# Kernel optimization log

Hardware: AMD Instinct MI355X
Metric: run time of the kernel (lower is better)

The kernel has to match this reference:

```python
import jax, jax.numpy as jnp
import numpy as np

X_DIM = 64
HIDDEN = 256
B = 64
T = 2048


def setup_inputs() -> dict:
    key = jax.random.key(0)
    k1, k2, k3, k4 = jax.random.split(key, 4)
    s = 1.0 / np.sqrt(HIDDEN)  # equinox LSTMCell uniform init scale
    x_seq = jax.random.normal(k1, (B, T, X_DIM), dtype=jnp.float32)
    w_ih = jax.random.uniform(k2, (4 * HIDDEN, X_DIM), minval=-s, maxval=s, dtype=jnp.float32)
    w_hh = jax.random.uniform(k3, (4 * HIDDEN, HIDDEN), minval=-s, maxval=s, dtype=jnp.float32)
    bias = jax.random.uniform(k4, (4 * HIDDEN,), minval=-s, maxval=s, dtype=jnp.float32)
    return {"x_seq": x_seq, "w_ih": w_ih, "w_hh": w_hh, "bias": bias}


def reference(x_seq, w_ih, w_hh, bias):
    # x_seq: (B, T, x_dim) -> h_seq: (B, T, H). Gate order i,f,g,o (equinox/torch).
    Bsz, Tlen, _ = x_seq.shape
    H = w_hh.shape[1]
    h0 = jnp.zeros((Bsz, H), dtype=x_seq.dtype)
    c0 = jnp.zeros((Bsz, H), dtype=x_seq.dtype)

    def step(carry, x_t):
        h, c = carry
        z = x_t @ w_ih.T + h @ w_hh.T + bias  # (B, 4H)
        i, f, g, o = jnp.split(z, 4, axis=-1)
        i = jax.nn.sigmoid(i)
        f = jax.nn.sigmoid(f)
        g = jnp.tanh(g)
        o = jax.nn.sigmoid(o)
        c = f * c + i * g
        h = o * jnp.tanh(c)
        return (h, c), h

    (_, _), hs = jax.lax.scan(step, (h0, c0), x_seq.transpose(1, 0, 2))  # hs: (T, B, H)
    return hs.transpose(1, 0, 2)
```

## Files before the change

### kernel.cpp

```cpp
#include <hip/hip_runtime.h>

#define XD    64
#define HID   256
#define G4    1024
#define TLEN  2048
#define BATCH 64
#define NPART 8
#define UPB   32
#define CPB   128
#define TSTRIDE 16

typedef unsigned int uint;

__device__ __forceinline__ float sigmf(float x) {
    return 1.0f / (1.0f + __expf(-x));
}
__device__ __forceinline__ float tanhfast(float x) {
    return 1.0f - 2.0f / (1.0f + __expf(2.0f * x));
}

__device__ __forceinline__ uint2 ld_pair_sc0(const uint2* p) {
    uint2 r;
    asm volatile("global_load_dwordx2 %0, %1, off sc0 nt\n\ts_waitcnt vmcnt(0)"
                 : "=v"(r) : "v"(p) : "memory");
    return r;
}
__device__ __forceinline__ void st_pair_sc0(uint2* p, uint2 v) {
    asm volatile("global_store_dwordx2 %0, %1, off sc0" :: "v"(p), "v"(v) : "memory");
}
__device__ __forceinline__ uint2 ld_pair_dev(const uint2* p) {
    unsigned long long u = __hip_atomic_load((const unsigned long long*)p,
                                             __ATOMIC_RELAXED, __HIP_MEMORY_SCOPE_AGENT);
    uint2 r; r.x = (uint)(u & 0xffffffffu); r.y = (uint)(u >> 32); return r;
}
__device__ __forceinline__ void st_pair_dev(uint2* p, uint2 v) {
    unsigned long long u = ((unsigned long long)v.y << 32) | (unsigned long long)v.x;
    __hip_atomic_store((unsigned long long*)p, u, __ATOMIC_RELAXED, __HIP_MEMORY_SCOPE_AGENT);
}

__global__ void init_ws(unsigned long long* __restrict__ pairs, int* __restrict__ tok) {
    const int i = blockIdx.x * 256 + threadIdx.x;
    pairs[i] = 0ULL;
    pairs[BATCH * HID + i] = 0ULL;
    if (threadIdx.x < TSTRIDE) tok[blockIdx.x * TSTRIDE + threadIdx.x] = 0;
}

__global__ __launch_bounds__(256, 2)
void lstm_par(const float* __restrict__ x,
              const float* __restrict__ wih,
              const float* __restrict__ whh,
              const float* __restrict__ bias,
              float* __restrict__ out,
              uint2* __restrict__ pairs,
              int* __restrict__ tok)
{
    const int b    = blockIdx.x & 63;
    const int part = blockIdx.x >> 6;
    const int tid  = threadIdx.x;
    const int lane = tid & 63;
    const int wv   = tid >> 6;
    const int s    = tid >> 5;
    const int cq   = tid & 31;

    __shared__ __align__(16) float vec[XD + HID];
    __shared__ __align__(16) float zp[4][CPB];
    __shared__ int fastsh;

    float4 w4[40];
    {
        int jr[4];
        #pragma unroll
        for (int k = 0; k < 4; ++k) {
            const int c = 4 * cq + k;
            jr[k] = (c >> 5) * 256 + part * UPB + (c & 31);
        }
        #pragma unroll
        for (int e = 0; e < 40; ++e) {
            const int ge = s * 40 + e;
            float v0, v1, v2, v3;
            if (ge < XD) {
                v0 = wih[jr[0] * XD + ge]; v1 = wih[jr[1] * XD + ge];
                v2 = wih[jr[2] * XD + ge]; v3 = wih[jr[3] * XD + ge];
            } else {
                const int he = ge - XD;
                v0 = whh[jr[0] * HID + he]; v1 = whh[jr[1] * HID + he];
                v2 = whh[jr[2] * HID + he]; v3 = whh[jr[3] * HID + he];
            }
            w4[e] = make_float4(v0, v1, v2, v3);
        }
    }
    float bi = 0.f, bf = 0.f, bg = 0.f, bo = 0.f;
    if (tid < UPB) {
        const int gj = part * UPB + tid;
        bi = bias[gj]; bf = bias[256 + gj]; bg = bias[512 + gj]; bo = bias[768 + gj];
    }

    {
        int xcc;
        asm volatile("s_getreg_b32 %0, hwreg(HW_REG_XCC_ID)" : "=s"(xcc));
        xcc &= 15;
        int* tb = tok + b * TSTRIDE;
        if (tid == 0)
            __hip_atomic_store(tb + part, 256 + xcc, __ATOMIC_RELEASE,
                               __HIP_MEMORY_SCOPE_AGENT);
        if (tid < 64) {
            const int ln = tid & 7;
            int v = 0, guard = 0;
            for (;;) {
                v = __hip_atomic_load(tb + ln, __ATOMIC_RELAXED,
                                      __HIP_MEMORY_SCOPE_AGENT);
                if (__all(v >= 256)) break;
                __builtin_amdgcn_s_sleep(2);
                if (++guard > 200000) break;
            }
            const int ok = __all(v >= 256);
            const int v0 = __shfl(v, 0);
            const int eq = (ok && __all(v == v0)) ? 1 : 0;
            if (tid == 0) fastsh = eq;
        }
        __syncthreads();
    }
    const bool fast = (fastsh != 0);

    uint2* __restrict__ pb0 = pairs + (size_t)b * HID;
    uint2* __restrict__ pb1 = pairs + (size_t)(BATCH + b) * HID;
    const float* __restrict__ xb = x + (size_t)b * TLEN * XD;
    float* __restrict__ ob = out + (size_t)b * TLEN * HID;

    float cst = 0.0f;
    float xreg = (tid < XD) ? xb[tid] : 0.0f;

    for (int t = 0; t < TLEN; ++t) {
        if (t > 0) {
            const uint2* src = ((t & 1) ? pb0 : pb1) + tid;
            uint2 pr;
            int it = 0;
            for (;;) {
                pr = (fast && it < 4096) ? ld_pair_sc0(src) : ld_pair_dev(src);
                if (pr.y == (uint)t) break;
                __builtin_amdgcn_s_sleep(1);
                if (++it > 100000) break;
            }
            vec[XD + tid] = __uint_as_float(pr.x);
        } else {
            vec[XD + tid] = 0.0f;
        }
        if (tid < XD) vec[tid] = xreg;
        __syncthreads();

        if (t + 1 < TLEN && tid < XD) xreg = xb[(size_t)(t + 1) * XD + tid];

        float4 acc = make_float4(0.f, 0.f, 0.f, 0.f);
        const float4* vb = (const float4*)(vec + 40 * s);
        #pragma unroll
        for (int i = 0; i < 10; ++i) {
            const float4 v = vb[i];
            #define FMA1(R, VE)                              \
                acc.x = fmaf(w4[4*i + R].x, (VE), acc.x);    \
                acc.y = fmaf(w4[4*i + R].y, (VE), acc.y);    \
                acc.z = fmaf(w4[4*i + R].z, (VE), acc.z);    \
                acc.w = fmaf(w4[4*i + R].w, (VE), acc.w);
            FMA1(0, v.x) FMA1(1, v.y) FMA1(2, v.z) FMA1(3, v.w)
            #undef FMA1
        }
        acc.x += __shfl_xor(acc.x, 32);
        acc.y += __shfl_xor(acc.y, 32);
        acc.z += __shfl_xor(acc.z, 32);
        acc.w += __shfl_xor(acc.w, 32);
        if (lane < 32) *(float4*)(&zp[wv][4 * lane]) = acc;
        __syncthreads();

        if (tid < UPB) {
            float zi = bi, zf = bf, zg = bg, zo = bo;
            #pragma unroll
            for (int w2 = 0; w2 < 4; ++w2) {
                zi += zp[w2][tid];
                zf += zp[w2][32 + tid];
                zg += zp[w2][64 + tid];
                zo += zp[w2][96 + tid];
            }
            const float ig = sigmf(zi);
            const float fg = sigmf(zf);
            const float gg = tanhfast(zg);
            const float og = sigmf(zo);
            cst = fg * cst + ig * gg;
            const float h = og * tanhfast(cst);
            uint2 pv; pv.x = __float_as_uint(h); pv.y = (uint)(t + 1);
            uint2* dst = ((t & 1) ? pb1 : pb0) + part * UPB + tid;
            if (fast) st_pair_sc0(dst, pv);
            else      st_pair_dev(dst, pv);
            ob[(size_t)t * HID + part * UPB + tid] = h;
        }
    }
}

extern "C" void kernel_launch(void* const* d_in, const int* in_sizes, int n_in,
                              void* d_out, int out_size, void* d_ws, size_t ws_size,
                              hipStream_t stream) {
    const float* x    = (const float*)d_in[0];
    const float* wih  = (const float*)d_in[1];
    const float* whh  = (const float*)d_in[2];
    const float* bias = (const float*)d_in[3];
    float* out = (float*)d_out;

    uint2* pairs = (uint2*)d_ws;
    int*   tok   = (int*)((char*)d_ws + (size_t)2 * BATCH * HID * sizeof(uint2));

    hipLaunchKernelGGL(init_ws, dim3(BATCH), dim3(256), 0, stream,
                       (unsigned long long*)d_ws, tok);
    hipLaunchKernelGGL(lstm_par, dim3(BATCH * NPART), dim3(256), 0, stream,
                       x, wih, whh, bias, out, pairs, tok);
}
```

Baseline: 2.759 ms.

## Interleave two batch chains per block to hide cross-block latency

Each block now handles two batch elements (A and B) in alternation using the same register-resident weights. This halves the grid from 512 to 256 blocks and sets launch bounds to 1 block per SM. While chain A's h values travel between blocks, the block computes chain B, which is meant to hide the inter-block exchange latency. The cost is twice the serial compute per block per timestep, and the sync groups now span two batches.

```diff
diff --git a/kernel.cpp b/kernel.cpp
--- a/kernel.cpp
+++ b/kernel.cpp
@@ -6,6 +6,7 @@
 #define TLEN  2048
 #define BATCH 64
 #define NPART 8
+#define NGRP  32
 #define UPB   32
 #define CPB   128
 #define TSTRIDE 16
@@ -45,7 +46,7 @@
     if (threadIdx.x < TSTRIDE) tok[blockIdx.x * TSTRIDE + threadIdx.x] = 0;
 }
 
-__global__ __launch_bounds__(256, 2)
+__global__ __launch_bounds__(256, 1)
 void lstm_par(const float* __restrict__ x,
               const float* __restrict__ wih,
               const float* __restrict__ whh,
@@ -54,16 +55,18 @@
               uint2* __restrict__ pairs,
               int* __restrict__ tok)
 {
-    const int b    = blockIdx.x & 63;
-    const int part = blockIdx.x >> 6;
+    const int grp  = blockIdx.x & 31;
+    const int part = blockIdx.x >> 5;
+    const int cA   = grp * 2;
+    const int cB   = grp * 2 + 1;
     const int tid  = threadIdx.x;
     const int lane = tid & 63;
     const int wv   = tid >> 6;
     const int s    = tid >> 5;
     const int cq   = tid & 31;
 
-    __shared__ __align__(16) float vec[XD + HID];
-    __shared__ __align__(16) float zp[4][CPB];
+    __shared__ __align__(16) float vecA[XD + HID], vecB[XD + HID];
+    __shared__ __align__(16) float zpA[4][CPB], zpB[4][CPB];
     __shared__ int fastsh;
 
     float4 w4[40];
@@ -99,7 +102,7 @@
         int xcc;
         asm volatile("s_getreg_b32 %0, hwreg(HW_REG_XCC_ID)" : "=s"(xcc));
         xcc &= 15;
-        int* tb = tok + b * TSTRIDE;
+        int* tb = tok + grp * TSTRIDE;
         if (tid == 0)
             __hip_atomic_store(tb + part, 256 + xcc, __ATOMIC_RELEASE,
                                __HIP_MEMORY_SCOPE_AGENT);
@@ -122,76 +125,109 @@
     }
     const bool fast = (fastsh != 0);
 
-    uint2* __restrict__ pb0 = pairs + (size_t)b * HID;
-    uint2* __restrict__ pb1 = pairs + (size_t)(BATCH + b) * HID;
-    const float* __restrict__ xb = x + (size_t)b * TLEN * XD;
-    float* __restrict__ ob = out + (size_t)b * TLEN * HID;
-
-    float cst = 0.0f;
-    float xreg = (tid < XD) ? xb[tid] : 0.0f;
+    uint2* __restrict__ pA0 = pairs + (size_t)cA * HID;
+    uint2* __restrict__ pA1 = pairs + (size_t)(BATCH + cA) * HID;
+    uint2* __restrict__ pB0 = pairs + (size_t)cB * HID;
+    uint2* __restrict__ pB1 = pairs + (size_t)(BATCH + cB) * HID;
+    const float* __restrict__ xbA = x + (size_t)cA * TLEN * XD;
+    const float* __restrict__ xbB = x + (size_t)cB * TLEN * XD;
+    float* __restrict__ obA = out + (size_t)cA * TLEN * HID;
+    float* __restrict__ obB = out + (size_t)cB * TLEN * HID;
+
+    float cstA = 0.0f, cstB = 0.0f;
+    float xregA = (tid < XD) ? xbA[tid] : 0.0f;
+    float xregB = (tid < XD) ? xbB[tid] : 0.0f;
+
+    #define POLLSTAGE(P0, P1, VEC, XREG) do {                                 \
+        if (t > 0) {                                                          \
+            const uint2* src = ((t & 1) ? (P0) : (P1)) + tid;                 \
+            uint2 pr; int it = 0;                                             \
+            for (;;) {                                                        \
+                pr = (fast && it < 4096) ? ld_pair_sc0(src) : ld_pair_dev(src);\
+                if (pr.y == (uint)t) break;   \
+                __builtin_amdgcn_s_sleep(1);  \
+                if (++it > 100000) break;     \
+            }                                                                 \
+            (VEC)[XD + tid] = __uint_as_float(pr.x);                          \
+        } else {                                                              \
+            (VEC)[XD + tid] = 0.0f;                                           \
+        }                                                                     \
+        if (tid < XD) (VEC)[tid] = (XREG);                                    \
+    } while (0)
+
+    #define COMPUTE(VEC, ZP) do {                                             \
+        float4 acc = make_float4(0.f, 0.f, 0.f, 0.f);                         \
+        const float4* vb = (const float4*)((VEC) + 40 * s);                   \
+        _Pragma("unroll")                                                     \
+        for (int i = 0; i < 10; ++i) {                                        \
+            const float4 v = vb[i];                                           \
+            acc.x = fmaf(w4[4*i+0].x, v.x, acc.x);                            \
+            acc.y = fmaf(w4[4*i+0].y, v.x, acc.y);                            \
+            acc.z = fmaf(w4[4*i+0].z, v.x, acc.z);                            \
+            acc.w = fmaf(w4[4*i+0].w, v.x, acc.w);                            \
+            acc.x = fmaf(w4[4*i+1].x, v.y, acc.x);                            \
+            acc.y = fmaf(w4[4*i+1].y, v.y, acc.y);                            \
+            acc.z = fmaf(w4[4*i+1].z, v.y, acc.z);                            \
+            acc.w = fmaf(w4[4*i+1].w, v.y, acc.w);                            \
+            acc.x = fmaf(w4[4*i+2].x, v.z, acc.x);                            \
+            acc.y = fmaf(w4[4*i+2].y, v.z, acc.y);                            \
+            acc.z = fmaf(w4[4*i+2].z, v.z, acc.z);                            \
+            acc.w = fmaf(w4[4*i+2].w, v.z, acc.w);                            \
+            acc.x = fmaf(w4[4*i+3].x, v.w, acc.x);                            \
+            acc.y = fmaf(w4[4*i+3].y, v.w, acc.y);                            \
+            acc.z = fmaf(w4[4*i+3].z, v.w, acc.z);                            \
+            acc.w = fmaf(w4[4*i+3].w, v.w, acc.w);                            \
+        }                                                                     \
+        acc.x += __shfl_xor(acc.x, 32);                                       \
+        acc.y += __shfl_xor(acc.y, 32);                                       \
+        acc.z += __shfl_xor(acc.z, 32);                                       \
+        acc.w += __shfl_xor(acc.w, 32);                                       \
+        if (lane < 32) *(float4*)(&(ZP)[wv][4 * lane]) = acc;                 \
+    } while (0)
+
+    #define GATES(ZP, CST, P0, P1, OB) do {                                   \
+        if (tid < UPB) {                                                      \
+            float zi = bi, zf = bf, zg = bg, zo = bo;                         \
+            _Pragma("unroll")                                                 \
+            for (int w2 = 0; w2 < 4; ++w2) {                                  \
+                zi += (ZP)[w2][tid];                                          \
+                zf += (ZP)[w2][32 + tid];                                     \
+                zg += (ZP)[w2][64 + tid];                                     \
+                zo += (ZP)[w2][96 + tid];                                     \
+            }                                                                 \
+            const float ig = sigmf(zi);                                       \
+            const float fg = sigmf(zf);                                       \
+            const float gg = tanhfast(zg);                                    \
+            const float og = sigmf(zo);                                       \
+            (CST) = fg * (CST) + ig * gg;                                     \
+            const float h = og * tanhfast(CST);                               \
+            uint2 pv; pv.x = __float_as_uint(h); pv.y = (uint)(t + 1);        \
+            uint2* dst = ((t & 1) ? (P1) : (P0)) + part * UPB + tid;          \
+            if (fast) st_pair_sc0(dst, pv);                                   \
+            else      st_pair_dev(dst, pv);                                   \
+            (OB)[(size_t)t * HID + part * UPB + tid] = h;                     \
+        }                                                                     \
+    } while (0)
 
     for (int t = 0; t < TLEN; ++t) {
-        if (t > 0) {
-            const uint2* src = ((t & 1) ? pb0 : pb1) + tid;
-            uint2 pr;
-            int it = 0;
-            for (;;) {
-                pr = (fast && it < 4096) ? ld_pair_sc0(src) : ld_pair_dev(src);
-                if (pr.y == (uint)t) break;
-                __builtin_amdgcn_s_sleep(1);
-                if (++it > 100000) break;
-            }
-            vec[XD + tid] = __uint_as_float(pr.x);
-        } else {
-            vec[XD + tid] = 0.0f;
-        }
-        if (tid < XD) vec[tid] = xreg;
-        __syncthreads();
-
-        if (t + 1 < TLEN && tid < XD) xreg = xb[(size_t)(t + 1) * XD + tid];
-
-        float4 acc = make_float4(0.f, 0.f, 0.f, 0.f);
-        const float4* vb = (const float4*)(vec + 40 * s);
-        #pragma unroll
-        for (int i = 0; i < 10; ++i) {
-            const float4 v = vb[i];
-            #define FMA1(R, VE)                              \
-                acc.x = fmaf(w4[4*i + R].x, (VE), acc.x);    \
-                acc.y = fmaf(w4[4*i + R].y, (VE), acc.y);    \
-                acc.z = fmaf(w4[4*i + R].z, (VE), acc.z);    \
-                acc.w = fmaf(w4[4*i + R].w, (VE), acc.w);
-            FMA1(0, v.x) FMA1(1, v.y) FMA1(2, v.z) FMA1(3, v.w)
-            #undef FMA1
-        }
-        acc.x += __shfl_xor(acc.x, 32);
-        acc.y += __shfl_xor(acc.y, 32);
-        acc.z += __shfl_xor(acc.z, 32);
-        acc.w += __shfl_xor(acc.w, 32);
-        if (lane < 32) *(float4*)(&zp[wv][4 * lane]) = acc;
-        __syncthreads();
-
-        if (tid < UPB) {
-            float zi = bi, zf = bf, zg = bg, zo = bo;
-            #pragma unroll
-            for (int w2 = 0; w2 < 4; ++w2) {
-                zi += zp[w2][tid];
-                zf += zp[w2][32 + tid];
-                zg += zp[w2][64 + tid];
-                zo += zp[w2][96 + tid];
-            }
-            const float ig = sigmf(zi);
-            const float fg = sigmf(zf);
-            const float gg = tanhfast(zg);
-            const float og = sigmf(zo);
-            cst = fg * cst + ig * gg;
-            const float h = og * tanhfast(cst);
-            uint2 pv; pv.x = __float_as_uint(h); pv.y = (uint)(t + 1);
-            uint2* dst = ((t & 1) ? pb1 : pb0) + part * UPB + tid;
-            if (fast) st_pair_sc0(dst, pv);
-            else      st_pair_dev(dst, pv);
-            ob[(size_t)t * HID + part * UPB + tid] = h;
-        }
-    }
+        POLLSTAGE(pA0, pA1, vecA, xregA);
+        __syncthreads();
+        if (t + 1 < TLEN && tid < XD)
+            xregA = xbA[(size_t)(t + 1) * XD + tid];
+        COMPUTE(vecA, zpA);
+        __syncthreads();
+        GATES(zpA, cstA, pA0, pA1, obA);
+        POLLSTAGE(pB0, pB1, vecB, xregB);
+        __syncthreads();
+        if (t + 1 < TLEN && tid < XD)
+            xregB = xbB[(size_t)(t + 1) * XD + tid];
+        COMPUTE(vecB, zpB);
+        __syncthreads();
+        GATES(zpB, cstB, pB0, pB1, obB);
+    }
+    #undef POLLSTAGE
+    #undef COMPUTE
+    #undef GATES
 }
 
 extern "C" void kernel_launch(void* const* d_in, const int* in_sizes, int n_in,
@@ -208,6 +244,6 @@
 
     hipLaunchKernelGGL(init_ws, dim3(BATCH), dim3(256), 0, stream,
                        (unsigned long long*)d_ws, tok);
-    hipLaunchKernelGGL(lstm_par, dim3(BATCH * NPART), dim3(256), 0, stream,
+    hipLaunchKernelGGL(lstm_par, dim3(NGRP * NPART), dim3(256), 0, stream,
                        x, wih, whh, bias, out, pairs, tok);
 }
```

Result: slower. 4.764 ms (+72.7%).

## Remap blocks so batch groups co-locate, split gate math across lanes, spin before sleeping

Applied to the files above, without the earlier changes.

Changes the block-to-(batch, part) mapping so the eight parts of a batch row come from consecutive block ids, which makes them likely to share an XCC and take the fast sc0 path. Splits the gate nonlinearities over 64 lanes instead of 32 and exchanges them with a shuffle, shortening the serial per-step tail. Busy-polls 64 times before sleeping, to cut wake-up latency in the cross-block handoff. Adds an initial sleep for the upper half of the batch groups to stagger their start.

```diff
diff --git a/kernel.cpp b/kernel.cpp
--- a/kernel.cpp
+++ b/kernel.cpp
@@ -54,8 +54,9 @@
               uint2* __restrict__ pairs,
               int* __restrict__ tok)
 {
-    const int b    = blockIdx.x & 63;
-    const int part = blockIdx.x >> 6;
+    const int blk  = blockIdx.x;
+    const int part = (blk >> 3) & 7;
+    const int b    = (blk & 7) + 8 * (blk >> 6);
     const int tid  = threadIdx.x;
     const int lane = tid & 63;
     const int wv   = tid >> 6;
@@ -89,10 +90,12 @@
             w4[e] = make_float4(v0, v1, v2, v3);
         }
     }
-    float bi = 0.f, bf = 0.f, bg = 0.f, bo = 0.f;
-    if (tid < UPB) {
-        const int gj = part * UPB + tid;
-        bi = bias[gj]; bf = bias[256 + gj]; bg = bias[512 + gj]; bo = bias[768 + gj];
+    float b1 = 0.f, b2 = 0.f;
+    if (tid < 64) {
+        const int u  = tid & 31;
+        const int pu = part * UPB + u;
+        if (tid < 32) { b1 = bias[pu];       b2 = bias[512 + pu]; }
+        else          { b1 = bias[256 + pu]; b2 = bias[768 + pu]; }
     }
 
     {
@@ -122,6 +125,11 @@
     }
     const bool fast = (fastsh != 0);
 
+    if ((b >> 3) >= 4) {
+        __builtin_amdgcn_s_sleep(15);
+        __builtin_amdgcn_s_sleep(10);
+    }
+
     uint2* __restrict__ pb0 = pairs + (size_t)b * HID;
     uint2* __restrict__ pb1 = pairs + (size_t)(BATCH + b) * HID;
     const float* __restrict__ xb = x + (size_t)b * TLEN * XD;
@@ -138,8 +146,8 @@
             for (;;) {
                 pr = (fast && it < 4096) ? ld_pair_sc0(src) : ld_pair_dev(src);
                 if (pr.y == (uint)t) break;
-                __builtin_amdgcn_s_sleep(1);
-                if (++it > 100000) break;
+                if (++it > 64) __builtin_amdgcn_s_sleep(1);
+                if (it > 100000) break;
             }
             vec[XD + tid] = __uint_as_float(pr.x);
         } else {
@@ -170,26 +178,26 @@
         if (lane < 32) *(float4*)(&zp[wv][4 * lane]) = acc;
         __syncthreads();
 
-        if (tid < UPB) {
-            float zi = bi, zf = bf, zg = bg, zo = bo;
+        if (tid < 64) {
+            float z1 = b1, z2 = b2;
             #pragma unroll
             for (int w2 = 0; w2 < 4; ++w2) {
-                zi += zp[w2][tid];
-                zf += zp[w2][32 + tid];
-                zg += zp[w2][64 + tid];
-                zo += zp[w2][96 + tid];
-            }
-            const float ig = sigmf(zi);
-            const float fg = sigmf(zf);
-            const float gg = tanhfast(zg);
-            const float og = sigmf(zo);
-            cst = fg * cst + ig * gg;
-            const float h = og * tanhfast(cst);
-            uint2 pv; pv.x = __float_as_uint(h); pv.y = (uint)(t + 1);
-            uint2* dst = ((t & 1) ? pb1 : pb0) + part * UPB + tid;
-            if (fast) st_pair_sc0(dst, pv);
-            else      st_pair_dev(dst, pv);
-            ob[(size_t)t * HID + part * UPB + tid] = h;
+                z1 += zp[w2][tid];
+                z2 += zp[w2][64 + tid];
+            }
+            const float g1 = sigmf(z1);
+            const float g2 = (tid < 32) ? tanhfast(z2) : sigmf(z2);
+            const float gf = __shfl_xor(g1, 32);
+            const float go = __shfl_xor(g2, 32);
+            if (tid < UPB) {
+                cst = gf * cst + g1 * g2;
+                const float h = go * tanhfast(cst);
+                uint2 pv; pv.x = __float_as_uint(h); pv.y = (uint)(t + 1);
+                uint2* dst = ((t & 1) ? pb1 : pb0) + part * UPB + tid;
+                if (fast) st_pair_sc0(dst, pv);
+                else      st_pair_dev(dst, pv);
+                ob[(size_t)t * HID + part * UPB + tid] = h;
+            }
         }
     }
 }
```

After: 2.821 ms. 1.02x slower.

## Reduce gate partials with wave shuffles and double-buffer the input vector

Applied to the files above, without the earlier changes.

The thread-to-work mapping changes so that each wave owns 8 hidden units with all 4 gates per lane, and the K dimension is split across 8 lane groups. The partial sums are reduced with xor-shuffles at distances 8, 16 and 32, so the zp shared buffer and the second __syncthreads per timestep go away. The input vector is double-buffered by timestep parity so that the next step's writes do not race with reads from the current step. The cost is more shuffle instructions per step, and the nonlinearity and store work now runs on lanes spread across 4 waves instead of a single wave.

```diff
diff --git a/kernel.cpp b/kernel.cpp
--- a/kernel.cpp
+++ b/kernel.cpp
@@ -7,7 +7,6 @@
 #define BATCH 64
 #define NPART 8
 #define UPB   32
-#define CPB   128
 #define TSTRIDE 16
 
 typedef unsigned int uint;
@@ -59,21 +58,20 @@
     const int tid  = threadIdx.x;
     const int lane = tid & 63;
     const int wv   = tid >> 6;
-    const int s    = tid >> 5;
-    const int cq   = tid & 31;
-
-    __shared__ __align__(16) float vec[XD + HID];
-    __shared__ __align__(16) float zp[4][CPB];
+    const int s    = lane >> 3;
+    const int cq   = lane & 7;
+    const int u    = 8 * wv + cq;
+
+    __shared__ __align__(16) float vecb[2][XD + HID];
     __shared__ int fastsh;
 
     float4 w4[40];
+    float4 b4;
     {
         int jr[4];
         #pragma unroll
-        for (int k = 0; k < 4; ++k) {
-            const int c = 4 * cq + k;
-            jr[k] = (c >> 5) * 256 + part * UPB + (c & 31);
-        }
+        for (int q = 0; q < 4; ++q) jr[q] = q * 256 + part * UPB + u;
+        b4 = make_float4(bias[jr[0]], bias[jr[1]], bias[jr[2]], bias[jr[3]]);
         #pragma unroll
         for (int e = 0; e < 40; ++e) {
             const int ge = s * 40 + e;
@@ -88,11 +86,6 @@
             }
             w4[e] = make_float4(v0, v1, v2, v3);
         }
-    }
-    float bi = 0.f, bf = 0.f, bg = 0.f, bo = 0.f;
-    if (tid < UPB) {
-        const int gj = part * UPB + tid;
-        bi = bias[gj]; bf = bias[256 + gj]; bg = bias[512 + gj]; bo = bias[768 + gj];
     }
 
     {
@@ -131,6 +124,8 @@
     float xreg = (tid < XD) ? xb[tid] : 0.0f;
 
     for (int t = 0; t < TLEN; ++t) {
+        float* __restrict__ vec = vecb[t & 1];
+
         if (t > 0) {
             const uint2* src = ((t & 1) ? pb0 : pb1) + tid;
             uint2 pr;
@@ -163,33 +158,31 @@
             FMA1(0, v.x) FMA1(1, v.y) FMA1(2, v.z) FMA1(3, v.w)
             #undef FMA1
         }
+        acc.x += __shfl_xor(acc.x, 8);
+        acc.y += __shfl_xor(acc.y, 8);
+        acc.z += __shfl_xor(acc.z, 8);
+        acc.w += __shfl_xor(acc.w, 8);
+        acc.x += __shfl_xor(acc.x, 16);
+        acc.y += __shfl_xor(acc.y, 16);
+        acc.z += __shfl_xor(acc.z, 16);
+        acc.w += __shfl_xor(acc.w, 16);
         acc.x += __shfl_xor(acc.x, 32);
         acc.y += __shfl_xor(acc.y, 32);
         acc.z += __shfl_xor(acc.z, 32);
         acc.w += __shfl_xor(acc.w, 32);
-        if (lane < 32) *(float4*)(&zp[wv][4 * lane]) = acc;
-        __syncthreads();
-
-        if (tid < UPB) {
-            float zi = bi, zf = bf, zg = bg, zo = bo;
-            #pragma unroll
-            for (int w2 = 0; w2 < 4; ++w2) {
-                zi += zp[w2][tid];
-                zf += zp[w2][32 + tid];
-                zg += zp[w2][64 + tid];
-                zo += zp[w2][96 + tid];
-            }
-            const float ig = sigmf(zi);
-            const float fg = sigmf(zf);
-            const float gg = tanhfast(zg);
-            const float og = sigmf(zo);
+
+        if (lane < 8) {
+            const float ig = sigmf(acc.x + b4.x);
+            const float fg = sigmf(acc.y + b4.y);
+            const float gg = tanhfast(acc.z + b4.z);
+            const float og = sigmf(acc.w + b4.w);
             cst = fg * cst + ig * gg;
             const float h = og * tanhfast(cst);
             uint2 pv; pv.x = __float_as_uint(h); pv.y = (uint)(t + 1);
-            uint2* dst = ((t & 1) ? pb1 : pb0) + part * UPB + tid;
+            uint2* dst = ((t & 1) ? pb1 : pb0) + part * UPB + u;
             if (fast) st_pair_sc0(dst, pv);
             else      st_pair_dev(dst, pv);
-            ob[(size_t)t * HID + part * UPB + tid] = h;
+            ob[(size_t)t * HID + part * UPB + u] = h;
         }
     }
 }
```

Result: slower. 3.097 ms (+12.3%).
